# Optimization experiments

Hardware: AMD Instinct MI355X
Metric: run time of the kernel (lower is better)

Reference implementation:

```python
import jax, jax.numpy as jnp
import numpy as np

T, B, DIM_IN, DIM_STATE, NUM_CLASSES = 256, 64, 256, 512, 10000


def setup_inputs() -> dict:
    key = jax.random.key(0)
    ks = jax.random.split(key, 6)
    inputs = jax.random.normal(ks[0], (T, B, DIM_IN), dtype=jnp.float32)
    labels = jax.random.uniform(ks[1], (T, B, NUM_CLASSES), dtype=jnp.float32)
    labels = labels / jnp.sum(labels, axis=-1, keepdims=True)  # soft label distributions
    initial_state = jnp.zeros((B, DIM_STATE), dtype=jnp.float32)
    initial_output = jnp.zeros((B, DIM_STATE), dtype=jnp.float32)
    # LSTM cell params: gates packed as [i, f, g, o]
    Wx = jax.random.normal(ks[2], (DIM_IN, 4 * DIM_STATE), dtype=jnp.float32) * (1.0 / np.sqrt(DIM_IN))
    Wh = jax.random.normal(ks[3], (DIM_STATE, 4 * DIM_STATE), dtype=jnp.float32) * (1.0 / np.sqrt(DIM_STATE))
    b = jnp.zeros((4 * DIM_STATE,), dtype=jnp.float32)
    # Final FC (softmax head) params
    Wo = jax.random.normal(ks[4], (DIM_STATE, NUM_CLASSES), dtype=jnp.float32) * (1.0 / np.sqrt(DIM_STATE))
    bo = jnp.zeros((NUM_CLASSES,), dtype=jnp.float32)
    return {"inputs": inputs, "labels": labels, "initial_state": initial_state,
            "initial_output": initial_output, "Wx": Wx, "Wh": Wh, "b": b, "Wo": Wo, "bo": bo}


def reference(inputs, labels, initial_state, initial_output, Wx, Wh, b, Wo, bo):
    def step(carry, x_t):
        h, c = carry  # h: [B, DIM_STATE] previous output; c: [B, DIM_STATE] cell state
        z = x_t @ Wx + h @ Wh + b  # [B, 4*DIM_STATE]
        i, f, g, o = jnp.split(z, 4, axis=-1)
        c = jax.nn.sigmoid(f) * c + jax.nn.sigmoid(i) * jnp.tanh(g)
        h = jax.nn.sigmoid(o) * jnp.tanh(c)
        return (h, c), h

    _, hs = jax.lax.scan(step, (initial_output, initial_state), inputs)  # hs: [T, B, DIM_STATE]
    logits = jnp.einsum('tbs,sc->tbc', hs, Wo) + bo  # [T, B, NUM_CLASSES]
    log_p = jax.nn.log_softmax(logits, axis=-1)
    predictions = jnp.exp(log_p)  # softmax probabilities
    # softmax_cross_entropy_with_logits per (t, b), then mean over all
    total_loss = -jnp.mean(jnp.sum(labels * log_p, axis=-1))
    return predictions, total_loss
```

## Files before the change

kernel.cpp:

```cpp
#include <hip/hip_runtime.h>
#include <hip/hip_bf16.h>
#include <math.h>

#define T_STEPS 256
#define BATCH 64
#define DIN 256
#define DSTATE 512
#define NGATE 2048
#define NCLS 10000
#define NCLS_PAD 10112
#define ROWS 16384
#define SCAN_BLOCKS 64
#define GROUP_BLOCKS 16
#define CHUNK_ROWS 4096

typedef __attribute__((ext_vector_type(8))) short bf16x8;
typedef __attribute__((ext_vector_type(4))) float f32x4;

__device__ inline unsigned short f2b(float x) {
    __hip_bfloat16 h = __float2bfloat16(x);
    return *(unsigned short*)&h;
}
__device__ inline float b2f(unsigned short u) {
    return __uint_as_float(((unsigned int)u) << 16);
}


__global__ void init_bar(unsigned* __restrict__ bar) {
    bar[blockIdx.x * 256 + threadIdx.x] = 0u;
}

__global__ void f32_to_bf16(const float* __restrict__ in, unsigned short* __restrict__ out, int n4) {
    int i = blockIdx.x * 256 + threadIdx.x;
    if (i >= n4) return;
    float4 v = *(const float4*)&in[i * 4];
    ushort4 o;
    o.x = f2b(v.x); o.y = f2b(v.y); o.z = f2b(v.z); o.w = f2b(v.w);
    *(ushort4*)&out[i * 4] = o;
}

__global__ void build_wT(const float* __restrict__ W, unsigned short* __restrict__ WT,
                         int kshift, int total) {
    int e = blockIdx.x * 256 + threadIdx.x;
    if (e >= total) return;
    int jp = e >> kshift;
    int k = e & ((1 << kshift) - 1);
    int s = jp >> 2, g = jp & 3;
    WT[e] = f2b(W[(size_t)k * NGATE + g * DSTATE + s]);
}

__global__ void build_bias(const float* __restrict__ b, float* __restrict__ bp) {
    int jp = blockIdx.x * 256 + threadIdx.x;
    if (jp >= NGATE) return;
    bp[jp] = b[(jp & 3) * DSTATE + (jp >> 2)];
}

__launch_bounds__(256)
__global__ void transpose_wo(const float* __restrict__ Wo, unsigned short* __restrict__ WoT) {
    __shared__ float tile[64][65];
    const int tid = threadIdx.x;
    const int n0 = blockIdx.x * 64, k0 = blockIdx.y * 64;
    #pragma unroll
    for (int r = 0; r < 16; ++r) {
        int k = (tid >> 6) + r * 4;
        int n = tid & 63;
        float v = (n0 + n < NCLS) ? Wo[(size_t)(k0 + k) * NCLS + n0 + n] : 0.f;
        tile[k][n] = v;
    }
    __syncthreads();
    #pragma unroll
    for (int r = 0; r < 16; ++r) {
        int n = (tid >> 6) + r * 4;
        int k = tid & 63;
        WoT[(size_t)(n0 + n) * DSTATE + k0 + k] = f2b(tile[k][n]);
    }
}

__launch_bounds__(256)
__global__ void zx_gemm(const unsigned short* __restrict__ Xb,
                        const unsigned short* __restrict__ WxT,
                        const float* __restrict__ bp,
                        unsigned short* __restrict__ ZxT) {
    __shared__ unsigned short As[64][264];
    __shared__ unsigned short Bs[128][264];
    __shared__ float zls[4][32][65];
    const int tid = threadIdx.x;
    const int t = blockIdx.x;
    const int n0 = blockIdx.y * 128;
    const int wave = tid >> 6, lane = tid & 63, mr = lane & 15, g = lane >> 4;

    #pragma unroll
    for (int r = 0; r < 8; ++r) {
        int c = r * 256 + tid; int row = c >> 5, q = c & 31;
        *(int4*)&As[row][q * 8] = *(const int4*)&Xb[((size_t)t * 64 + row) * DIN + q * 8];
    }
    #pragma unroll
    for (int r = 0; r < 16; ++r) {
        int c = r * 256 + tid; int row = c >> 5, q = c & 31;
        *(int4*)&Bs[row][q * 8] = *(const int4*)&WxT[(size_t)(n0 + row) * DIN + q * 8];
    }
    __syncthreads();

    f32x4 acc[4][2] = {};
    #pragma unroll
    for (int kt = 0; kt < DIN; kt += 32) {
        bf16x8 af[4], bf[2];
        #pragma unroll
        for (int fm = 0; fm < 4; ++fm) af[fm] = *(const bf16x8*)&As[fm * 16 + mr][kt + g * 8];
        #pragma unroll
        for (int fn = 0; fn < 2; ++fn) bf[fn] = *(const bf16x8*)&Bs[wave * 32 + fn * 16 + mr][kt + g * 8];
        #pragma unroll
        for (int fm = 0; fm < 4; ++fm)
            #pragma unroll
            for (int fn = 0; fn < 2; ++fn)
                acc[fm][fn] = __builtin_amdgcn_mfma_f32_16x16x32_bf16(af[fm], bf[fn], acc[fm][fn], 0, 0, 0);
    }
    #pragma unroll
    for (int fm = 0; fm < 4; ++fm)
        #pragma unroll
        for (int fn = 0; fn < 2; ++fn)
            #pragma unroll
            for (int r = 0; r < 4; ++r)
                zls[wave][fn * 16 + mr][fm * 16 + g * 4 + r] = acc[fm][fn][r];
    #pragma unroll 4
    for (int jr = 0; jr < 32; ++jr) {
        int j = n0 + wave * 32 + jr;
        float v = zls[wave][jr][lane] + bp[j];
        ZxT[((size_t)t * NGATE + j) * 64 + lane] = f2b(v);
    }
}

__device__ __forceinline__ void groupbar(unsigned* fbase, int w, unsigned want, int tid) {
    __syncthreads();
    if (tid == 0)
        __hip_atomic_store(&fbase[w * 16], want, __ATOMIC_RELEASE, __HIP_MEMORY_SCOPE_AGENT);
    if (tid < GROUP_BLOCKS) {
        while (__hip_atomic_load(&fbase[tid * 16], __ATOMIC_RELAXED, __HIP_MEMORY_SCOPE_AGENT) < want) {}
        (void)__hip_atomic_load(&fbase[tid * 16], __ATOMIC_ACQUIRE, __HIP_MEMORY_SCOPE_AGENT);
    }
    __syncthreads();
}

__launch_bounds__(256, 1)
__global__ void lstm_scan_mfma(const unsigned short* __restrict__ h0b,
                               const float* __restrict__ c0,
                               const unsigned short* __restrict__ WhT,
                               const unsigned short* __restrict__ ZxT,
                               unsigned short* __restrict__ hsb,
                               unsigned* __restrict__ bar) {
    __shared__ unsigned short Wl[128][520];
    __shared__ unsigned short hT[16][520];
    __shared__ float zb[16][132];
    const int tid = threadIdx.x;
    const int bid = blockIdx.x;
    const int grp = bid >> 4;
    const int w   = bid & 15;
    const int b0  = grp * 16;
    const int j0  = w * 128;
    const int s0  = w * 32;
    const int wave = tid >> 6, lane = tid & 63, mr = lane & 15, gl = lane >> 4;
    unsigned* fbase = bar + grp * 256;

    #pragma unroll 4
    for (int r = 0; r < 32; ++r) {
        int c = r * 256 + tid; int row = c >> 6, q = c & 63;
        *(int4*)&Wl[row][q * 8] = *(const int4*)&WhT[(size_t)(j0 + row) * DSTATE + q * 8];
    }

    const int gb  = lane >> 2;
    const int slg = wave * 8 + (lane & 3) * 2;
    float creg0 = c0[(b0 + gb) * DSTATE + s0 + slg];
    float creg1 = c0[(b0 + gb) * DSTATE + s0 + slg + 1];
    __syncthreads();

    const size_t zo0 = ((size_t)(j0 + wave * 32 + mr)) * 64 + b0 + gl * 4;
    const size_t zo1 = ((size_t)(j0 + wave * 32 + 16 + mr)) * 64 + b0 + gl * 4;
    ushort4 za0 = *(const ushort4*)&ZxT[zo0];
    ushort4 za1 = *(const ushort4*)&ZxT[zo1];

    for (int t = 0; t < T_STEPS; ++t) {
        const unsigned short* hsrc = t ? (hsb + (size_t)(t - 1) * BATCH * DSTATE) : h0b;
        #pragma unroll
        for (int r = 0; r < 4; ++r) {
            int c = r * 256 + tid; int row = c >> 6, q = c & 63;
            *(int4*)&hT[row][q * 8] = *(const int4*)&hsrc[(size_t)(b0 + row) * DSTATE + q * 8];
        }
        __syncthreads();

        f32x4 acc0, acc1;
        acc0[0] = b2f(za0.x); acc0[1] = b2f(za0.y); acc0[2] = b2f(za0.z); acc0[3] = b2f(za0.w);
        acc1[0] = b2f(za1.x); acc1[1] = b2f(za1.y); acc1[2] = b2f(za1.z); acc1[3] = b2f(za1.w);
        if (t + 1 < T_STEPS) {
            za0 = *(const ushort4*)&ZxT[(size_t)(t + 1) * NGATE * 64 + zo0];
            za1 = *(const ushort4*)&ZxT[(size_t)(t + 1) * NGATE * 64 + zo1];
        }
        #pragma unroll
        for (int kt = 0; kt < DSTATE; kt += 32) {
            bf16x8 af = *(const bf16x8*)&hT[mr][kt + gl * 8];
            acc0 = __builtin_amdgcn_mfma_f32_16x16x32_bf16(af, *(const bf16x8*)&Wl[wave * 32 + mr][kt + gl * 8], acc0, 0, 0, 0);
            acc1 = __builtin_amdgcn_mfma_f32_16x16x32_bf16(af, *(const bf16x8*)&Wl[wave * 32 + 16 + mr][kt + gl * 8], acc1, 0, 0, 0);
        }
        #pragma unroll
        for (int r = 0; r < 4; ++r) {
            zb[gl * 4 + r][wave * 32 + mr] = acc0[r];
            zb[gl * 4 + r][wave * 32 + 16 + mr] = acc1[r];
        }
        {
            float zi0 = zb[gb][slg * 4 + 0], zf0 = zb[gb][slg * 4 + 1];
            float zg0 = zb[gb][slg * 4 + 2], zo0v = zb[gb][slg * 4 + 3];
            float zi1 = zb[gb][slg * 4 + 4], zf1 = zb[gb][slg * 4 + 5];
            float zg1 = zb[gb][slg * 4 + 6], zo1v = zb[gb][slg * 4 + 7];
            float i0 = 1.f / (1.f + expf(-zi0)), f0 = 1.f / (1.f + expf(-zf0));
            float o0 = 1.f / (1.f + expf(-zo0v)), g0 = tanhf(zg0);
            float i1 = 1.f / (1.f + expf(-zi1)), f1 = 1.f / (1.f + expf(-zf1));
            float o1 = 1.f / (1.f + expf(-zo1v)), g1 = tanhf(zg1);
            creg0 = f0 * creg0 + i0 * g0;
            creg1 = f1 * creg1 + i1 * g1;
            float h0v = o0 * tanhf(creg0);
            float h1v = o1 * tanhf(creg1);
            ushort2 hv; hv.x = f2b(h0v); hv.y = f2b(h1v);
            *(ushort2*)&hsb[((size_t)t * BATCH + b0 + gb) * DSTATE + s0 + slg] = hv;
        }
        if (t != T_STEPS - 1)
            groupbar(fbase, w, (unsigned)(t + 1), tid);
    }
}

__launch_bounds__(256)
__global__ void gemm_logits_bf16(const unsigned short* __restrict__ A,
                                 const unsigned short* __restrict__ Bt,
                                 const float* __restrict__ bo,
                                 unsigned short* __restrict__ Cb) {
    __shared__ unsigned short As[128 * 32];
    __shared__ unsigned short Bs[128 * 32];
    const int tid = threadIdx.x;
    const int wave = tid >> 6, lane = tid & 63;
    const int wm = wave >> 1, wn = wave & 1;
    const int m0 = blockIdx.y * 128, n0 = blockIdx.x * 128;
    const int g = lane >> 4, mr = lane & 15;

    const int ch0 = wave * 64 + lane;
    const int ch1 = (4 + wave) * 64 + lane;
    const int row0 = ch0 >> 2, q0 = ch0 & 3;
    const int row1 = ch1 >> 2, q1 = ch1 & 3;

    f32x4 acc[4][4] = {};
    for (int kt = 0; kt < DSTATE; kt += 32) {
        __builtin_amdgcn_global_load_lds(
            (const __attribute__((address_space(1))) void*)&A[(size_t)(m0 + row0) * DSTATE + kt + q0 * 8],
            (__attribute__((address_space(3))) void*)&As[ch0 * 8 - lane * 8], 16, 0, 0);
        __builtin_amdgcn_global_load_lds(
            (const __attribute__((address_space(1))) void*)&A[(size_t)(m0 + row1) * DSTATE + kt + q1 * 8],
            (__attribute__((address_space(3))) void*)&As[ch1 * 8 - lane * 8], 16, 0, 0);
        __builtin_amdgcn_global_load_lds(
            (const __attribute__((address_space(1))) void*)&Bt[(size_t)(n0 + row0) * DSTATE + kt + q0 * 8],
            (__attribute__((address_space(3))) void*)&Bs[ch0 * 8 - lane * 8], 16, 0, 0);
        __builtin_amdgcn_global_load_lds(
            (const __attribute__((address_space(1))) void*)&Bt[(size_t)(n0 + row1) * DSTATE + kt + q1 * 8],
            (__attribute__((address_space(3))) void*)&Bs[ch1 * 8 - lane * 8], 16, 0, 0);
        __syncthreads();

        bf16x8 af[4], bf[4];
        #pragma unroll
        for (int f = 0; f < 4; ++f) {
            af[f] = *(const bf16x8*)&As[(wm * 64 + f * 16 + mr) * 32 + g * 8];
            bf[f] = *(const bf16x8*)&Bs[(wn * 64 + f * 16 + mr) * 32 + g * 8];
        }
        #pragma unroll
        for (int fm = 0; fm < 4; ++fm)
            #pragma unroll
            for (int fn = 0; fn < 4; ++fn)
                acc[fm][fn] = __builtin_amdgcn_mfma_f32_16x16x32_bf16(af[fm], bf[fn], acc[fm][fn], 0, 0, 0);
        __syncthreads();
    }
    #pragma unroll
    for (int fm = 0; fm < 4; ++fm) {
        #pragma unroll
        for (int fn = 0; fn < 4; ++fn) {
            int col = n0 + wn * 64 + fn * 16 + mr;
            if (col >= NCLS) continue;
            float bias = bo[col];
            #pragma unroll
            for (int r = 0; r < 4; ++r) {
                int row = m0 + wm * 64 + fm * 16 + g * 4 + r;
                Cb[(size_t)row * NCLS + col] = f2b(acc[fm][fn][r] + bias);
            }
        }
    }
}

__launch_bounds__(256)
__global__ void gemm_logits_mfma(const unsigned short* __restrict__ A,
                                 const unsigned short* __restrict__ Bt,
                                 const float* __restrict__ bo,
                                 float* __restrict__ C) {
    __shared__ unsigned short As[128 * 32];
    __shared__ unsigned short Bs[128 * 32];
    const int tid = threadIdx.x;
    const int wave = tid >> 6, lane = tid & 63;
    const int wm = wave >> 1, wn = wave & 1;
    const int m0 = blockIdx.y * 128, n0 = blockIdx.x * 128;
    const int g = lane >> 4, mr = lane & 15;

    const int ch0 = wave * 64 + lane;
    const int ch1 = (4 + wave) * 64 + lane;
    const int row0 = ch0 >> 2, q0 = ch0 & 3;
    const int row1 = ch1 >> 2, q1 = ch1 & 3;

    f32x4 acc[4][4] = {};
    for (int kt = 0; kt < DSTATE; kt += 32) {
        __builtin_amdgcn_global_load_lds(
            (const __attribute__((address_space(1))) void*)&A[(size_t)(m0 + row0) * DSTATE + kt + q0 * 8],
            (__attribute__((address_space(3))) void*)&As[ch0 * 8 - lane * 8], 16, 0, 0);
        __builtin_amdgcn_global_load_lds(
            (const __attribute__((address_space(1))) void*)&A[(size_t)(m0 + row1) * DSTATE + kt + q1 * 8],
            (__attribute__((address_space(3))) void*)&As[ch1 * 8 - lane * 8], 16, 0, 0);
        __builtin_amdgcn_global_load_lds(
            (const __attribute__((address_space(1))) void*)&Bt[(size_t)(n0 + row0) * DSTATE + kt + q0 * 8],
            (__attribute__((address_space(3))) void*)&Bs[ch0 * 8 - lane * 8], 16, 0, 0);
        __builtin_amdgcn_global_load_lds(
            (const __attribute__((address_space(1))) void*)&Bt[(size_t)(n0 + row1) * DSTATE + kt + q1 * 8],
            (__attribute__((address_space(3))) void*)&Bs[ch1 * 8 - lane * 8], 16, 0, 0);
        __syncthreads();

        bf16x8 af[4], bf[4];
        #pragma unroll
        for (int f = 0; f < 4; ++f) {
            af[f] = *(const bf16x8*)&As[(wm * 64 + f * 16 + mr) * 32 + g * 8];
            bf[f] = *(const bf16x8*)&Bs[(wn * 64 + f * 16 + mr) * 32 + g * 8];
        }
        #pragma unroll
        for (int fm = 0; fm < 4; ++fm)
            #pragma unroll
            for (int fn = 0; fn < 4; ++fn)
                acc[fm][fn] = __builtin_amdgcn_mfma_f32_16x16x32_bf16(af[fm], bf[fn], acc[fm][fn], 0, 0, 0);
        __syncthreads();
    }
    #pragma unroll
    for (int fm = 0; fm < 4; ++fm) {
        #pragma unroll
        for (int fn = 0; fn < 4; ++fn) {
            int col = n0 + wn * 64 + fn * 16 + mr;
            if (col >= NCLS) continue;
            float bias = bo[col];
            #pragma unroll
            for (int r = 0; r < 4; ++r) {
                int row = m0 + wm * 64 + fm * 16 + g * 4 + r;
                C[(size_t)row * NCLS + col] = acc[fm][fn][r] + bias;
            }
        }
    }
}

__device__ inline float wave_reduce_max(float v) {
    #pragma unroll
    for (int off = 32; off > 0; off >>= 1) v = fmaxf(v, __shfl_xor(v, off));
    return v;
}
__device__ inline float wave_reduce_sum(float v) {
    #pragma unroll
    for (int off = 32; off > 0; off >>= 1) v += __shfl_xor(v, off);
    return v;
}

__launch_bounds__(256)
__global__ void softmax_loss_bf16(const unsigned short* __restrict__ Cb,
                                  const float* __restrict__ labels,
                                  float* __restrict__ probs,
                                  float* __restrict__ rowloss) {
    __shared__ float row[NCLS];
    __shared__ float sm[4];
    const int tid = threadIdx.x;
    const size_t base = (size_t)blockIdx.x * NCLS;

    float m = -INFINITY;
    for (int c8 = tid; c8 < NCLS / 8; c8 += 256) {
        ushort4 u0 = *(const ushort4*)&Cb[base + c8 * 8];
        ushort4 u1 = *(const ushort4*)&Cb[base + c8 * 8 + 4];
        float v0 = b2f(u0.x), v1 = b2f(u0.y), v2 = b2f(u0.z), v3 = b2f(u0.w);
        float v4 = b2f(u1.x), v5 = b2f(u1.y), v6 = b2f(u1.z), v7 = b2f(u1.w);
        float4 a = {v0, v1, v2, v3}, b = {v4, v5, v6, v7};
        *(float4*)&row[c8 * 8] = a;
        *(float4*)&row[c8 * 8 + 4] = b;
        m = fmaxf(m, fmaxf(fmaxf(fmaxf(v0, v1), fmaxf(v2, v3)),
                           fmaxf(fmaxf(v4, v5), fmaxf(v6, v7))));
    }
    m = wave_reduce_max(m);
    if ((tid & 63) == 0) sm[tid >> 6] = m;
    __syncthreads();
    m = fmaxf(fmaxf(sm[0], sm[1]), fmaxf(sm[2], sm[3]));
    __syncthreads();

    float s = 0.f, dot = 0.f;
    for (int c4 = tid; c4 < NCLS / 4; c4 += 256) {
        float4 v = *(const float4*)&row[c4 * 4];
        float4 lb = *(const float4*)&labels[base + c4 * 4];
        s += expf(v.x - m) + expf(v.y - m) + expf(v.z - m) + expf(v.w - m);
        dot += lb.x * v.x + lb.y * v.y + lb.z * v.z + lb.w * v.w;
    }
    s = wave_reduce_sum(s);
    if ((tid & 63) == 0) sm[tid >> 6] = s;
    __syncthreads();
    s = sm[0] + sm[1] + sm[2] + sm[3];
    __syncthreads();
    dot = wave_reduce_sum(dot);
    if ((tid & 63) == 0) sm[tid >> 6] = dot;
    __syncthreads();
    dot = sm[0] + sm[1] + sm[2] + sm[3];

    float inv = 1.f / s;
    for (int c4 = tid; c4 < NCLS / 4; c4 += 256) {
        float4 v = *(const float4*)&row[c4 * 4];
        float4 o;
        o.x = expf(v.x - m) * inv; o.y = expf(v.y - m) * inv;
        o.z = expf(v.z - m) * inv; o.w = expf(v.w - m) * inv;
        *(float4*)&probs[base + c4 * 4] = o;
    }
    if (tid == 0) rowloss[blockIdx.x] = (m + logf(s)) - dot;
}

__launch_bounds__(256)
__global__ void softmax_loss(float* __restrict__ logits,
                             const float* __restrict__ labels,
                             float* __restrict__ rowloss) {
    __shared__ float row[NCLS];
    __shared__ float sm[4];
    const int tid = threadIdx.x;
    const size_t base = (size_t)blockIdx.x * NCLS;

    float m = -INFINITY;
    for (int c4 = tid; c4 < NCLS / 4; c4 += 256) {
        float4 v = *(const float4*)&logits[base + c4 * 4];
        *(float4*)&row[c4 * 4] = v;
        m = fmaxf(fmaxf(m, fmaxf(v.x, v.y)), fmaxf(v.z, v.w));
    }
    m = wave_reduce_max(m);
    if ((tid & 63) == 0) sm[tid >> 6] = m;
    __syncthreads();
    m = fmaxf(fmaxf(sm[0], sm[1]), fmaxf(sm[2], sm[3]));
    __syncthreads();

    float s = 0.f, dot = 0.f;
    for (int c4 = tid; c4 < NCLS / 4; c4 += 256) {
        float4 v = *(const float4*)&row[c4 * 4];
        float4 lb = *(const float4*)&labels[base + c4 * 4];
        s += expf(v.x - m) + expf(v.y - m) + expf(v.z - m) + expf(v.w - m);
        dot += lb.x * v.x + lb.y * v.y + lb.z * v.z + lb.w * v.w;
    }
    s = wave_reduce_sum(s);
    if ((tid & 63) == 0) sm[tid >> 6] = s;
    __syncthreads();
    s = sm[0] + sm[1] + sm[2] + sm[3];
    __syncthreads();
    dot = wave_reduce_sum(dot);
    if ((tid & 63) == 0) sm[tid >> 6] = dot;
    __syncthreads();
    dot = sm[0] + sm[1] + sm[2] + sm[3];

    float inv = 1.f / s;
    for (int c4 = tid; c4 < NCLS / 4; c4 += 256) {
        float4 v = *(const float4*)&row[c4 * 4];
        float4 o;
        o.x = expf(v.x - m) * inv; o.y = expf(v.y - m) * inv;
        o.z = expf(v.z - m) * inv; o.w = expf(v.w - m) * inv;
        *(float4*)&logits[base + c4 * 4] = o;
    }
    if (tid == 0) rowloss[blockIdx.x] = (m + logf(s)) - dot;
}

__launch_bounds__(256)
__global__ void loss_reduce(const float* __restrict__ rowloss, float* __restrict__ out) {
    __shared__ float sm[4];
    float s = 0.f;
    for (int i = threadIdx.x; i < ROWS; i += 256) s += rowloss[i];
    s = wave_reduce_sum(s);
    if ((threadIdx.x & 63) == 0) sm[threadIdx.x >> 6] = s;
    __syncthreads();
    if (threadIdx.x == 0) out[0] = (sm[0] + sm[1] + sm[2] + sm[3]) * (1.f / ROWS);
}

extern "C" void kernel_launch(void* const* d_in, const int* in_sizes, int n_in,
                              void* d_out, int out_size, void* d_ws, size_t ws_size,
                              hipStream_t stream) {
    const float* inputs = (const float*)d_in[0];
    const float* labels = (const float*)d_in[1];
    const float* c0     = (const float*)d_in[2];
    const float* h0     = (const float*)d_in[3];
    const float* Wx     = (const float*)d_in[4];
    const float* Wh     = (const float*)d_in[5];
    const float* bias   = (const float*)d_in[6];
    const float* Wo     = (const float*)d_in[7];
    const float* bo     = (const float*)d_in[8];
    float* out = (float*)d_out;

    float* ws = (float*)d_ws;
    float* bp       = ws;
    float* rowloss  = bp + 2048;
    unsigned short* WhT = (unsigned short*)(rowloss + 16384);
    unsigned short* WxT = WhT + 1048576;
    unsigned short* Xb  = WxT + 524288;
    unsigned short* h0b = Xb + 4194304;
    unsigned short* hsb = h0b + 32768;
    unsigned short* WoT = hsb + 8388608;
    unsigned short* ZxT = WoT + 5177344;
    unsigned* bar = (unsigned*)(ZxT + 33554432);
    unsigned short* Cb = (unsigned short*)(bar + 1024);

    size_t base_bytes = (size_t)((char*)Cb - (char*)d_ws);
    size_t need_bf16 = base_bytes + (size_t)CHUNK_ROWS * NCLS * sizeof(unsigned short);
    bool use_bf16 = (ws_size >= need_bf16);

    init_bar<<<4, 256, 0, stream>>>(bar);
    f32_to_bf16<<<(ROWS * DIN / 4 + 255) / 256, 256, 0, stream>>>(inputs, Xb, ROWS * DIN / 4);
    f32_to_bf16<<<(BATCH * DSTATE / 4 + 255) / 256, 256, 0, stream>>>(h0, h0b, BATCH * DSTATE / 4);
    build_wT<<<(NGATE * DSTATE + 255) / 256, 256, 0, stream>>>(Wh, WhT, 9, NGATE * DSTATE);
    build_wT<<<(NGATE * DIN + 255) / 256, 256, 0, stream>>>(Wx, WxT, 8, NGATE * DIN);
    build_bias<<<(NGATE + 255) / 256, 256, 0, stream>>>(bias, bp);
    transpose_wo<<<dim3(NCLS_PAD / 64, DSTATE / 64), 256, 0, stream>>>(Wo, WoT);

    zx_gemm<<<dim3(T_STEPS, NGATE / 128), 256, 0, stream>>>(Xb, WxT, bp, ZxT);

    void* args[] = {(void*)&h0b, (void*)&c0, (void*)&WhT, (void*)&ZxT, (void*)&hsb, (void*)&bar};
    hipLaunchCooperativeKernel((const void*)lstm_scan_mfma, dim3(SCAN_BLOCKS), dim3(256),
                               args, 0, stream);

    if (use_bf16) {
        for (int row0 = 0; row0 < ROWS; row0 += CHUNK_ROWS) {
            gemm_logits_bf16<<<dim3(NCLS_PAD / 128, CHUNK_ROWS / 128), 256, 0, stream>>>(
                hsb + (size_t)row0 * DSTATE, WoT, bo, Cb);
            softmax_loss_bf16<<<CHUNK_ROWS, 256, 0, stream>>>(
                Cb, labels + (size_t)row0 * NCLS, out + (size_t)row0 * NCLS, rowloss + row0);
        }
    } else {
        gemm_logits_mfma<<<dim3(NCLS_PAD / 128, ROWS / 128), 256, 0, stream>>>(hsb, WoT, bo, out);
        softmax_loss<<<ROWS, 256, 0, stream>>>(out, labels, rowloss);
    }
    loss_reduce<<<1, 256, 0, stream>>>(rowloss, out + (size_t)ROWS * NCLS);
}
```

Measured before the change: 1.959 ms.

## Merge prep kernels, stage logits stores through LDS, widen softmax blocks

Folds seven small preprocessing launches into one kernel whose work is dispatched by block-index range, removing per-launch overhead. The bf16 logits GEMM now writes its tile to shared memory and then stores 16-byte coalesced rows instead of scattered 2-byte writes. The softmax/loss kernel goes from 256 to 512 threads per row to expose more parallelism. The GEMM change adds about 34KB of LDS per block, which may lower occupancy.

```diff
diff --git a/kernel.cpp b/kernel.cpp
--- a/kernel.cpp
+++ b/kernel.cpp
@@ -25,54 +25,61 @@
     return __uint_as_float(((unsigned int)u) << 16);
 }
 
-
-__global__ void init_bar(unsigned* __restrict__ bar) {
-    bar[blockIdx.x * 256 + threadIdx.x] = 0u;
-}
-
-__global__ void f32_to_bf16(const float* __restrict__ in, unsigned short* __restrict__ out, int n4) {
-    int i = blockIdx.x * 256 + threadIdx.x;
-    if (i >= n4) return;
-    float4 v = *(const float4*)&in[i * 4];
-    ushort4 o;
-    o.x = f2b(v.x); o.y = f2b(v.y); o.z = f2b(v.z); o.w = f2b(v.w);
-    *(ushort4*)&out[i * 4] = o;
-}
-
-__global__ void build_wT(const float* __restrict__ W, unsigned short* __restrict__ WT,
-                         int kshift, int total) {
-    int e = blockIdx.x * 256 + threadIdx.x;
-    if (e >= total) return;
-    int jp = e >> kshift;
-    int k = e & ((1 << kshift) - 1);
-    int s = jp >> 2, g = jp & 3;
-    WT[e] = f2b(W[(size_t)k * NGATE + g * DSTATE + s]);
-}
-
-__global__ void build_bias(const float* __restrict__ b, float* __restrict__ bp) {
-    int jp = blockIdx.x * 256 + threadIdx.x;
-    if (jp >= NGATE) return;
-    bp[jp] = b[(jp & 3) * DSTATE + (jp >> 2)];
-}
-
 __launch_bounds__(256)
-__global__ void transpose_wo(const float* __restrict__ Wo, unsigned short* __restrict__ WoT) {
+__global__ void prep_all(const float* __restrict__ inputs, const float* __restrict__ Wx,
+                         const float* __restrict__ Wh, const float* __restrict__ bias,
+                         const float* __restrict__ h0, const float* __restrict__ Wo,
+                         unsigned short* __restrict__ Xb, unsigned short* __restrict__ WxT,
+                         unsigned short* __restrict__ WhT, float* __restrict__ bp,
+                         unsigned short* __restrict__ h0b, unsigned* __restrict__ bar,
+                         unsigned short* __restrict__ WoT) {
     __shared__ float tile[64][65];
-    const int tid = threadIdx.x;
-    const int n0 = blockIdx.x * 64, k0 = blockIdx.y * 64;
-    #pragma unroll
-    for (int r = 0; r < 16; ++r) {
-        int k = (tid >> 6) + r * 4;
-        int n = tid & 63;
-        float v = (n0 + n < NCLS) ? Wo[(size_t)(k0 + k) * NCLS + n0 + n] : 0.f;
-        tile[k][n] = v;
-    }
-    __syncthreads();
-    #pragma unroll
-    for (int r = 0; r < 16; ++r) {
-        int n = (tid >> 6) + r * 4;
-        int k = tid & 63;
-        WoT[(size_t)(n0 + n) * DSTATE + k0 + k] = f2b(tile[k][n]);
+    const int bid = blockIdx.x;
+    const int tid = threadIdx.x;
+    if (bid < 4096) {
+        int i = bid * 256 + tid;
+        float4 v = *(const float4*)&inputs[(size_t)i * 4];
+        ushort4 o; o.x = f2b(v.x); o.y = f2b(v.y); o.z = f2b(v.z); o.w = f2b(v.w);
+        *(ushort4*)&Xb[(size_t)i * 4] = o;
+    } else if (bid < 8192) {
+        int e = (bid - 4096) * 256 + tid;
+        int jp = e >> 9, k = e & 511;
+        int s = jp >> 2, g = jp & 3;
+        WhT[e] = f2b(Wh[(size_t)k * NGATE + g * DSTATE + s]);
+    } else if (bid < 10240) {
+        int e = (bid - 8192) * 256 + tid;
+        int jp = e >> 8, k = e & 255;
+        int s = jp >> 2, g = jp & 3;
+        WxT[e] = f2b(Wx[(size_t)k * NGATE + g * DSTATE + s]);
+    } else if (bid < 10248) {
+        int jp = (bid - 10240) * 256 + tid;
+        if (jp < NGATE) bp[jp] = bias[(jp & 3) * DSTATE + (jp >> 2)];
+    } else if (bid < 10280) {
+        int i = (bid - 10248) * 256 + tid;
+        if (i < BATCH * DSTATE / 4) {
+            float4 v = *(const float4*)&h0[(size_t)i * 4];
+            ushort4 o; o.x = f2b(v.x); o.y = f2b(v.y); o.z = f2b(v.z); o.w = f2b(v.w);
+            *(ushort4*)&h0b[(size_t)i * 4] = o;
+        }
+    } else if (bid < 10284) {
+        bar[(bid - 10280) * 256 + tid] = 0u;
+    } else {
+        int nb = bid - 10284;
+        int n0 = (nb % 158) * 64, k0 = (nb / 158) * 64;
+        #pragma unroll
+        for (int r = 0; r < 16; ++r) {
+            int k = (tid >> 6) + r * 4;
+            int n = tid & 63;
+            float v = (n0 + n < NCLS) ? Wo[(size_t)(k0 + k) * NCLS + n0 + n] : 0.f;
+            tile[k][n] = v;
+        }
+        __syncthreads();
+        #pragma unroll
+        for (int r = 0; r < 16; ++r) {
+            int n = (tid >> 6) + r * 4;
+            int k = tid & 63;
+            WoT[(size_t)(n0 + n) * DSTATE + k0 + k] = f2b(tile[k][n]);
+        }
     }
 }
 
@@ -233,6 +240,7 @@
                                  unsigned short* __restrict__ Cb) {
     __shared__ unsigned short As[128 * 32];
     __shared__ unsigned short Bs[128 * 32];
+    __shared__ unsigned short sC[128][136];
     const int tid = threadIdx.x;
     const int wave = tid >> 6, lane = tid & 63;
     const int wm = wave >> 1, wn = wave & 1;
@@ -274,18 +282,23 @@
         __syncthreads();
     }
     #pragma unroll
-    for (int fm = 0; fm < 4; ++fm) {
-        #pragma unroll
-        for (int fn = 0; fn < 4; ++fn) {
-            int col = n0 + wn * 64 + fn * 16 + mr;
-            if (col >= NCLS) continue;
-            float bias = bo[col];
+    for (int fn = 0; fn < 4; ++fn) {
+        int colg = n0 + wn * 64 + fn * 16 + mr;
+        float bias = (colg < NCLS) ? bo[colg] : 0.f;
+        #pragma unroll
+        for (int fm = 0; fm < 4; ++fm)
             #pragma unroll
-            for (int r = 0; r < 4; ++r) {
-                int row = m0 + wm * 64 + fm * 16 + g * 4 + r;
-                Cb[(size_t)row * NCLS + col] = f2b(acc[fm][fn][r] + bias);
-            }
-        }
+            for (int r = 0; r < 4; ++r)
+                sC[wm * 64 + fm * 16 + g * 4 + r][wn * 64 + fn * 16 + mr] = f2b(acc[fm][fn][r] + bias);
+    }
+    __syncthreads();
+    #pragma unroll
+    for (int rr = 0; rr < 8; ++rr) {
+        int row_l = (tid >> 4) + rr * 16;
+        int col0 = (tid & 15) * 8;
+        int gcol = n0 + col0;
+        if (gcol < NCLS)
+            *(int4*)&Cb[(size_t)(m0 + row_l) * NCLS + gcol] = *(int4*)&sC[row_l][col0];
     }
 }
 
@@ -363,18 +376,18 @@
     return v;
 }
 
-__launch_bounds__(256)
+__launch_bounds__(512)
 __global__ void softmax_loss_bf16(const unsigned short* __restrict__ Cb,
                                   const float* __restrict__ labels,
                                   float* __restrict__ probs,
                                   float* __restrict__ rowloss) {
     __shared__ float row[NCLS];
-    __shared__ float sm[4];
+    __shared__ float sm[8];
     const int tid = threadIdx.x;
     const size_t base = (size_t)blockIdx.x * NCLS;
 
     float m = -INFINITY;
-    for (int c8 = tid; c8 < NCLS / 8; c8 += 256) {
+    for (int c8 = tid; c8 < NCLS / 8; c8 += 512) {
         ushort4 u0 = *(const ushort4*)&Cb[base + c8 * 8];
         ushort4 u1 = *(const ushort4*)&Cb[base + c8 * 8 + 4];
         float v0 = b2f(u0.x), v1 = b2f(u0.y), v2 = b2f(u0.z), v3 = b2f(u0.w);
@@ -388,11 +401,12 @@
     m = wave_reduce_max(m);
     if ((tid & 63) == 0) sm[tid >> 6] = m;
     __syncthreads();
-    m = fmaxf(fmaxf(sm[0], sm[1]), fmaxf(sm[2], sm[3]));
+    m = fmaxf(fmaxf(fmaxf(sm[0], sm[1]), fmaxf(sm[2], sm[3])),
+              fmaxf(fmaxf(sm[4], sm[5]), fmaxf(sm[6], sm[7])));
     __syncthreads();
 
     float s = 0.f, dot = 0.f;
-    for (int c4 = tid; c4 < NCLS / 4; c4 += 256) {
+    for (int c4 = tid; c4 < NCLS / 4; c4 += 512) {
         float4 v = *(const float4*)&row[c4 * 4];
         float4 lb = *(const float4*)&labels[base + c4 * 4];
         s += expf(v.x - m) + expf(v.y - m) + expf(v.z - m) + expf(v.w - m);
@@ -401,15 +415,15 @@
     s = wave_reduce_sum(s);
     if ((tid & 63) == 0) sm[tid >> 6] = s;
     __syncthreads();
-    s = sm[0] + sm[1] + sm[2] + sm[3];
+    s = ((sm[0] + sm[1]) + (sm[2] + sm[3])) + ((sm[4] + sm[5]) + (sm[6] + sm[7]));
     __syncthreads();
     dot = wave_reduce_sum(dot);
     if ((tid & 63) == 0) sm[tid >> 6] = dot;
     __syncthreads();
-    dot = sm[0] + sm[1] + sm[2] + sm[3];
+    dot = ((sm[0] + sm[1]) + (sm[2] + sm[3])) + ((sm[4] + sm[5]) + (sm[6] + sm[7]));
 
     float inv = 1.f / s;
-    for (int c4 = tid; c4 < NCLS / 4; c4 += 256) {
+    for (int c4 = tid; c4 < NCLS / 4; c4 += 512) {
         float4 v = *(const float4*)&row[c4 * 4];
         float4 o;
         o.x = expf(v.x - m) * inv; o.y = expf(v.y - m) * inv;
@@ -510,13 +524,8 @@
     size_t need_bf16 = base_bytes + (size_t)CHUNK_ROWS * NCLS * sizeof(unsigned short);
     bool use_bf16 = (ws_size >= need_bf16);
 
-    init_bar<<<4, 256, 0, stream>>>(bar);
-    f32_to_bf16<<<(ROWS * DIN / 4 + 255) / 256, 256, 0, stream>>>(inputs, Xb, ROWS * DIN / 4);
-    f32_to_bf16<<<(BATCH * DSTATE / 4 + 255) / 256, 256, 0, stream>>>(h0, h0b, BATCH * DSTATE / 4);
-    build_wT<<<(NGATE * DSTATE + 255) / 256, 256, 0, stream>>>(Wh, WhT, 9, NGATE * DSTATE);
-    build_wT<<<(NGATE * DIN + 255) / 256, 256, 0, stream>>>(Wx, WxT, 8, NGATE * DIN);
-    build_bias<<<(NGATE + 255) / 256, 256, 0, stream>>>(bias, bp);
-    transpose_wo<<<dim3(NCLS_PAD / 64, DSTATE / 64), 256, 0, stream>>>(Wo, WoT);
+    prep_all<<<11548, 256, 0, stream>>>(inputs, Wx, Wh, bias, h0, Wo,
+                                        Xb, WxT, WhT, bp, h0b, bar, WoT);
 
     zx_gemm<<<dim3(T_STEPS, NGATE / 128), 256, 0, stream>>>(Xb, WxT, bp, ZxT);
 
@@ -528,7 +537,7 @@
         for (int row0 = 0; row0 < ROWS; row0 += CHUNK_ROWS) {
             gemm_logits_bf16<<<dim3(NCLS_PAD / 128, CHUNK_ROWS / 128), 256, 0, stream>>>(
                 hsb + (size_t)row0 * DSTATE, WoT, bo, Cb);
-            softmax_loss_bf16<<<CHUNK_ROWS, 256, 0, stream>>>(
+            softmax_loss_bf16<<<CHUNK_ROWS, 512, 0, stream>>>(
                 Cb, labels + (size_t)row0 * NCLS, out + (size_t)row0 * NCLS, rowloss + row0);
         }
     } else {
```

Measured after the change: 1.893 ms, median of 2. 1.03x faster.
